# Optimization experiments

Hardware: AMD Instinct MI355X
Metric: run time of the kernel (lower is better)

The kernel has to match this reference:

```python
import jax, jax.numpy as jnp
import numpy as np

H = 256
L = 3
LN_EPS = 1e-5


def _layernorm(z, g, b):
    mu = jnp.mean(z, axis=-1, keepdims=True)
    var = jnp.mean(jnp.square(z - mu), axis=-1, keepdims=True)
    return (z - mu) / jnp.sqrt(var + LN_EPS) * g + b


def setup_inputs() -> dict:
    key = jax.random.key(0)
    ks = jax.random.split(key, 32)
    B, n = 32, 1024
    N = B * n
    E = 16 * N
    node_in, edge_in = 3, 4
    s = 0.05
    inp = {
        'x': jax.random.normal(ks[0], (N, node_in), jnp.float32),
        'edge_attr': jax.random.normal(ks[1], (E, edge_in), jnp.float32),
        'edge_index': jax.random.randint(ks[2], (2, E), 0, N, jnp.int64),
        'a': jax.random.randint(ks[3], (B, n), 0, 2, jnp.int32),
        # node_proj: Linear(node_in+1 -> H)
        'np_w': jax.random.normal(ks[4], (node_in + 1, H), jnp.float32) * s,
        'np_b': jnp.zeros((H,), jnp.float32),
        # edge_mlp: Linear(edge_in->H), ReLU, Linear(H->H)
        'em_w1': jax.random.normal(ks[5], (edge_in, H), jnp.float32) * s,
        'em_b1': jnp.zeros((H,), jnp.float32),
        'em_w2': jax.random.normal(ks[6], (H, H), jnp.float32) * s,
        'em_b2': jnp.zeros((H,), jnp.float32),
        # per-layer GINEConv internal edge lin (edge_dim=H -> H)
        'lin_w': jax.random.normal(ks[7], (L, H, H), jnp.float32) * s,
        'lin_b': jnp.zeros((L, H), jnp.float32),
        # per-layer GINEConv nn: Linear(H->H), ReLU, Linear(H->H)
        'm_w1': jax.random.normal(ks[8], (L, H, H), jnp.float32) * s,
        'm_b1': jnp.zeros((L, H), jnp.float32),
        'm_w2': jax.random.normal(ks[9], (L, H, H), jnp.float32) * s,
        'm_b2': jnp.zeros((L, H), jnp.float32),
        # per-layer LayerNorm
        'ln_g': jnp.ones((L, H), jnp.float32),
        'ln_b': jnp.zeros((L, H), jnp.float32),
        # head: Linear(H->H), ReLU, Linear(H->1)
        'hd_w1': jax.random.normal(ks[10], (H, H), jnp.float32) * s,
        'hd_b1': jnp.zeros((H,), jnp.float32),
        'hd_w2': jax.random.normal(ks[11], (H, 1), jnp.float32) * s,
        'hd_b2': jnp.zeros((1,), jnp.float32),
    }
    return inp


def reference(x, edge_attr, edge_index, a,
              np_w, np_b, em_w1, em_b1, em_w2, em_b2,
              lin_w, lin_b, m_w1, m_b1, m_w2, m_b2, ln_g, ln_b,
              hd_w1, hd_b1, hd_w2, hd_b2):
    N = x.shape[0]
    B, n = a.shape
    # graphs are packed contiguously: batch = i//n, local = i%n ->
    # a[batch, local] == a.reshape(-1)
    a_s = a.reshape(-1).astype(x.dtype)[:, None]            # [N,1]
    h = jax.nn.relu(jnp.concatenate([x, a_s], -1) @ np_w + np_b)  # [N,H]
    e = jax.nn.relu(edge_attr @ em_w1 + em_b1) @ em_w2 + em_b2    # [E,H]
    src, dst = edge_index[0], edge_index[1]
    for l in range(L):
        e_l = e @ lin_w[l] + lin_b[l]                       # GINEConv edge lin
        msg = jax.nn.relu(h[src] + e_l)                     # [E,H]
        agg = jax.ops.segment_sum(msg, dst, num_segments=N) # scatter-add
        z = h + agg                                          # (1+eps)*h, eps=0
        z = jax.nn.relu(z @ m_w1[l] + m_b1[l]) @ m_w2[l] + m_b2[l]
        z = _layernorm(z, ln_g[l], ln_b[l])
        h = h + jax.nn.relu(z)                              # residual
    batch_vec = jnp.arange(N) // n
    g = jax.ops.segment_sum(h, batch_vec, num_segments=B) / n  # mean pool
    q = (jax.nn.relu(g @ hd_w1 + hd_b1) @ hd_w2 + hd_b2)[:, 0]
    return q
```

## Files before the change

kernel.cpp:

```cpp
#include <hip/hip_runtime.h>
#include <hip/hip_bf16.h>

#define H 256
#define LN_EPS 1e-5f
#define PITCH 264
#define TE 128

typedef __attribute__((ext_vector_type(8))) short bf16x8;
typedef __attribute__((ext_vector_type(4))) float f32x4;

__device__ __forceinline__ float bf2f(unsigned short u) {
  union { unsigned int i; float f; } v; v.i = ((unsigned int)u) << 16; return v.f;
}
__device__ __forceinline__ unsigned short f2bf(float f) {
  union { float f; unsigned int i; } v; v.f = f;
  unsigned int x = v.i;
  return (unsigned short)((x + 0x7fffu + ((x >> 16) & 1u)) >> 16);
}
__device__ __forceinline__ unsigned int pack2bf(float a, float b) {
  __hip_bfloat162 t = __float22bfloat162_rn(make_float2(a, b));
  unsigned int u;
  __builtin_memcpy(&u, &t, 4);
  return u;
}
__device__ __forceinline__ unsigned short f2bf1(float a) {
  return (unsigned short)pack2bf(a, a);
}
__device__ __forceinline__ void fsplit(float v, unsigned short& hi, unsigned short& lo) {
  hi = f2bf(v);
  lo = f2bf(v - bf2f(hi));
}

__device__ __forceinline__ void gemm_tile(const float* __restrict__ sA,
                                          const float* __restrict__ W,
                                          int lane_j, int rg, float acc[8][4]) {
#pragma unroll
  for (int mm = 0; mm < 8; mm++)
#pragma unroll
    for (int cc = 0; cc < 4; cc++) acc[mm][cc] = 0.f;
  for (int k = 0; k < H; k += 4) {
    float tvf[8][4];
#pragma unroll
    for (int mm = 0; mm < 8; mm++)
      *(float4*)&tvf[mm][0] = *(const float4*)&sA[(rg * 8 + mm) * H + k];
#pragma unroll
    for (int kk = 0; kk < 4; kk++) {
      const float* wr = W + (k + kk) * H + lane_j;
      float w0 = wr[0], w1 = wr[64], w2 = wr[128], w3 = wr[192];
#pragma unroll
      for (int mm = 0; mm < 8; mm++) {
        float av = tvf[mm][kk];
        acc[mm][0] = fmaf(av, w0, acc[mm][0]);
        acc[mm][1] = fmaf(av, w1, acc[mm][1]);
        acc[mm][2] = fmaf(av, w2, acc[mm][2]);
        acc[mm][3] = fmaf(av, w3, acc[mm][3]);
      }
    }
  }
}


__global__ void k_detect(const int* __restrict__ ei, int* __restrict__ flag) {
  if (threadIdx.x == 0 && blockIdx.x == 0)
    *flag = (ei[1] == 0 && ei[3] == 0 && ei[5] == 0 && ei[7] == 0) ? 1 : 0;
}

__global__ __launch_bounds__(256) void k_zero(float4* __restrict__ p, int n4) {
  int i = blockIdx.x * 256 + threadIdx.x;
  if (i < n4) p[i] = make_float4(0.f, 0.f, 0.f, 0.f);
}

__global__ __launch_bounds__(256) void k_hist(
    const void* __restrict__ ei, const int* __restrict__ flag64,
    int* __restrict__ hist, int E) {
  int e = blockIdx.x * 256 + threadIdx.x;
  if (e >= E) return;
  int d = (*flag64) ? (int)((const long long*)ei)[(size_t)E + e]
                    : ((const int*)ei)[(size_t)E + e];
  atomicAdd(&hist[d], 1);
}

__global__ __launch_bounds__(256) void k_scan(
    const int* __restrict__ hist, int* __restrict__ cursor, int N) {
  __shared__ int part[256];
  int tid = threadIdx.x;
  int chunk = (N + 255) / 256;
  int s = 0;
  for (int i = 0; i < chunk; i++) {
    int idx = tid * chunk + i;
    if (idx < N) s += hist[idx];
  }
  part[tid] = s;
  __syncthreads();
  for (int off = 1; off < 256; off <<= 1) {
    int v = (tid >= off) ? part[tid - off] : 0;
    __syncthreads();
    part[tid] += v;
    __syncthreads();
  }
  int excl = (tid == 0) ? 0 : part[tid - 1];
  for (int i = 0; i < chunk; i++) {
    int idx = tid * chunk + i;
    if (idx < N) {
      cursor[idx] = excl;
      excl += hist[idx];
    }
  }
}

__global__ __launch_bounds__(256) void k_scatter(
    const void* __restrict__ ei, const int* __restrict__ flag64,
    const float* __restrict__ ea, int* __restrict__ cursor,
    int* __restrict__ srcS, int* __restrict__ dstS, float* __restrict__ eaS, int E) {
  int e = blockIdx.x * 256 + threadIdx.x;
  if (e >= E) return;
  int is64 = *flag64;
  int s = is64 ? (int)((const long long*)ei)[e] : ((const int*)ei)[e];
  int d = is64 ? (int)((const long long*)ei)[(size_t)E + e]
               : ((const int*)ei)[(size_t)E + e];
  int p = atomicAdd(&cursor[d], 1);
  srcS[p] = s;
  dstS[p] = d;
  ((float4*)eaS)[p] = ((const float4*)ea)[e];
}

__global__ __launch_bounds__(256) void k_node_proj(
    const float* __restrict__ x, const int* __restrict__ a,
    const float* __restrict__ w, const float* __restrict__ b,
    float* __restrict__ h, unsigned short* __restrict__ hbf, int N) {
  int node = blockIdx.x;
  int j = threadIdx.x;
  float acc = b[j];
  acc = fmaf(x[node * 3 + 0], w[0 * H + j], acc);
  acc = fmaf(x[node * 3 + 1], w[1 * H + j], acc);
  acc = fmaf(x[node * 3 + 2], w[2 * H + j], acc);
  acc = fmaf((float)a[node], w[3 * H + j], acc);
  float v = fmaxf(acc, 0.f);
  h[(size_t)node * H + j] = v;
  hbf[(size_t)node * H + j] = f2bf1(v);
}

__global__ __launch_bounds__(256, 2) void k_wcomb(
    const float* __restrict__ w2, const float* __restrict__ lin_w,
    unsigned short* __restrict__ wcTh, unsigned short* __restrict__ wcTl) {
  __shared__ __align__(16) float sA[32 * H];
  int l = blockIdx.x >> 3, tile = blockIdx.x & 7;
  int tid = threadIdx.x;
  const float4* src = (const float4*)(w2 + (size_t)tile * 32 * H);
#pragma unroll
  for (int it = 0; it < 8; it++) {
    int vi = it * 256 + tid;
    *(float4*)&sA[vi * 4] = src[vi];
  }
  __syncthreads();
  int lane_j = tid & 63, rg = tid >> 6;
  float acc[8][4];
  gemm_tile(sA, lin_w + (size_t)l * H * H, lane_j, rg, acc);
  unsigned short* oh = wcTh + (size_t)l * H * H;
  unsigned short* ol = wcTl + (size_t)l * H * H;
#pragma unroll
  for (int cc = 0; cc < 4; cc++) {
    int j = lane_j + 64 * cc;
#pragma unroll
    for (int mm = 0; mm < 8; mm++) {
      int k = tile * 32 + rg * 8 + mm;
      unsigned short hi, lo;
      fsplit(acc[mm][cc], hi, lo);
      oh[(size_t)j * H + k] = hi;
      ol[(size_t)j * H + k] = lo;
    }
  }
}

__global__ __launch_bounds__(256) void k_beta(
    const float* __restrict__ lin_w, const float* __restrict__ lin_b,
    const float* __restrict__ b2, float* __restrict__ beta) {
  int l = blockIdx.x, j = threadIdx.x;
  const float* W = lin_w + (size_t)l * H * H;
  float v = lin_b[l * H + j];
  for (int k = 0; k < H; k++) v = fmaf(b2[k], W[k * H + j], v);
  beta[l * H + j] = v;
}

__global__ __launch_bounds__(256) void k_transp(
    const float* __restrict__ in,
    unsigned short* __restrict__ outh, unsigned short* __restrict__ outl) {
  int l = blockIdx.z;
  int kb = blockIdx.x * 64, nb = blockIdx.y * 64;
  int tid = threadIdx.x;
  __shared__ float T[64][65];
  const float* src = in + (size_t)l * H * H;
#pragma unroll
  for (int it = 0; it < 16; it++) {
    int idx = it * 256 + tid;
    int kl = idx >> 6, nl = idx & 63;
    T[kl][nl] = src[(size_t)(kb + kl) * H + nb + nl];
  }
  __syncthreads();
  unsigned short* dh = outh + (size_t)l * H * H;
  unsigned short* dl = outl + (size_t)l * H * H;
#pragma unroll
  for (int it = 0; it < 8; it++) {
    int u = it * 256 + tid;
    int nl = u >> 5, k2 = (u & 31) * 2;
    unsigned short h0, l0, h1, l1;
    fsplit(T[k2][nl], h0, l0);
    fsplit(T[k2 + 1][nl], h1, l1);
    size_t o = (size_t)(nb + nl) * H + kb + k2;
    *(unsigned int*)&dh[o] = (unsigned int)h0 | ((unsigned int)h1 << 16);
    *(unsigned int*)&dl[o] = (unsigned int)l0 | ((unsigned int)l1 << 16);
  }
}


__global__ __launch_bounds__(1024, 8) void k_edge_mfma(
    const float* __restrict__ eaS,
    const float* __restrict__ w1, const float* __restrict__ b1,
    const unsigned short* __restrict__ Wth,
    const float* __restrict__ beta,
    const unsigned short* __restrict__ hbf, float* __restrict__ agg,
    const int* __restrict__ srcS, const int* __restrict__ dstS) {
  __shared__ __align__(16) unsigned short sAh[TE * PITCH];
  __shared__ __align__(16) float sEA[TE * 4];
  __shared__ int sSrc[TE];
  __shared__ int sDst[TE];
  int tid = threadIdx.x;
  int base = blockIdx.x * TE;
  if (tid < TE) {
    sSrc[tid] = srcS[base + tid];
  } else if (tid < 2 * TE) {
    sDst[tid - TE] = dstS[base + tid - TE];
  } else if (tid < 3 * TE) {
    int t = tid - 2 * TE;
    ((float4*)sEA)[t] = ((const float4*)(eaS + (size_t)base * 4))[t];
  }
  __syncthreads();
  {
    int j2 = (tid & 127) * 2;
    int r0 = (tid >> 7) * 16;
    float wv0[4], wv1[4];
#pragma unroll
    for (int q = 0; q < 4; q++) { wv0[q] = w1[q * H + j2]; wv1[q] = w1[q * H + j2 + 1]; }
    float bb0 = b1[j2], bb1 = b1[j2 + 1];
#pragma unroll
    for (int m = r0; m < r0 + 16; m++) {
      float t0 = bb0, t1 = bb1;
#pragma unroll
      for (int q = 0; q < 4; q++) {
        float eav = sEA[m * 4 + q];
        t0 = fmaf(eav, wv0[q], t0);
        t1 = fmaf(eav, wv1[q], t1);
      }
      *(unsigned int*)&sAh[m * PITCH + j2] = pack2bf(fmaxf(t0, 0.f), fmaxf(t1, 0.f));
    }
  }
  __syncthreads();
  int lane = tid & 63, wv = tid >> 6;
  int lane15 = lane & 15, quad = lane >> 4;
  f32x4 acc[8];
#pragma unroll
  for (int i = 0; i < 8; i++) acc[i] = (f32x4){0.f, 0.f, 0.f, 0.f};
  const unsigned short* aph = sAh + lane15 * PITCH + quad * 8;
  const unsigned short* bph = Wth + (size_t)(wv * 16 + lane15) * H + quad * 8;
#pragma unroll
  for (int st = 0; st < 8; st++) {
    bf16x8 bhf = *(const bf16x8*)(bph + st * 32);
#pragma unroll
    for (int rg = 0; rg < 8; rg++) {
      bf16x8 ah = *(const bf16x8*)(aph + rg * 16 * PITCH + st * 32);
      acc[rg] = __builtin_amdgcn_mfma_f32_16x16x32_bf16(ah, bhf, acc[rg], 0, 0, 0);
    }
  }
  float bv = beta[wv * 16 + lane15];
  __syncthreads();
#pragma unroll
  for (int rg = 0; rg < 8; rg++) {
#pragma unroll
    for (int r = 0; r < 4; r++) {
      int row = rg * 16 + quad * 4 + r;
      sAh[row * PITCH + wv * 16 + lane15] = f2bf1(acc[rg][r] + bv);
    }
  }
  int jcol2 = (tid & 127) * 2, grp = tid >> 7;
  const int* msrc = sSrc + grp * 16;
  unsigned int hvp[16];
#pragma unroll
  for (int m = 0; m < 16; m++)
    hvp[m] = *(const unsigned int*)&hbf[(size_t)msrc[m] * H + jcol2];
  __syncthreads();
  {
    const int* mdst = sDst + grp * 16;
    float run0 = 0.f, run1 = 0.f;
    int prev = mdst[0];
#pragma unroll
    for (int m = 0; m < 16; m++) {
      int d = mdst[m];
      unsigned int hp = hvp[m];
      unsigned int ev = *(const unsigned int*)&sAh[(grp * 16 + m) * PITCH + jcol2];
      if (d != prev) {
        atomicAdd(&agg[(size_t)prev * H + jcol2], run0);
        atomicAdd(&agg[(size_t)prev * H + jcol2 + 1], run1);
        run0 = 0.f; run1 = 0.f;
        prev = d;
      }
      run0 += fmaxf(bf2f((unsigned short)hp) + bf2f((unsigned short)ev), 0.f);
      run1 += fmaxf(bf2f((unsigned short)(hp >> 16)) + bf2f((unsigned short)(ev >> 16)), 0.f);
    }
    atomicAdd(&agg[(size_t)prev * H + jcol2], run0);
    atomicAdd(&agg[(size_t)prev * H + jcol2 + 1], run1);
  }
}

__global__ __launch_bounds__(1024, 8) void k_node_mfma(
    float* __restrict__ h, unsigned short* __restrict__ hbf,
    float* __restrict__ agg,
    const unsigned short* __restrict__ w1Th, const float* __restrict__ b1,
    const unsigned short* __restrict__ w2Th, const float* __restrict__ b2,
    const float* __restrict__ lng, const float* __restrict__ lnb) {
  __shared__ __align__(16) unsigned short sAh[64 * PITCH];
  __shared__ float sPartS[64][16];
  __shared__ float sPartQ[64][16];
  __shared__ float sMu[64];
  __shared__ float sRstd[64];
  int tid = threadIdx.x;
  int base = blockIdx.x * 64;
  const float4* h4 = (const float4*)(h + (size_t)base * H);
  float4* a4 = (float4*)(agg + (size_t)base * H);
#pragma unroll
  for (int it = 0; it < 4; it++) {
    int vi = it * 1024 + tid;
    int row = vi >> 6, c4 = (vi & 63) * 4;
    float4 hv = h4[vi], av = a4[vi];
    a4[vi] = make_float4(0.f, 0.f, 0.f, 0.f);
    uint2 uh;
    uh.x = pack2bf(hv.x + av.x, hv.y + av.y);
    uh.y = pack2bf(hv.z + av.z, hv.w + av.w);
    *(uint2*)&sAh[row * PITCH + c4] = uh;
  }
  __syncthreads();
  int lane = tid & 63, wv = tid >> 6;
  int lane15 = lane & 15, quad = lane >> 4;
  int col = wv * 16 + lane15;
  const unsigned short* aph = sAh + lane15 * PITCH + quad * 8;
  f32x4 acc[4];
#pragma unroll
  for (int i = 0; i < 4; i++) acc[i] = (f32x4){0.f, 0.f, 0.f, 0.f};
  {
    const unsigned short* bph = w1Th + (size_t)col * H + quad * 8;
#pragma unroll
    for (int st = 0; st < 8; st++) {
      bf16x8 bhf = *(const bf16x8*)(bph + st * 32);
#pragma unroll
      for (int rg = 0; rg < 4; rg++) {
        bf16x8 ah = *(const bf16x8*)(aph + rg * 16 * PITCH + st * 32);
        acc[rg] = __builtin_amdgcn_mfma_f32_16x16x32_bf16(ah, bhf, acc[rg], 0, 0, 0);
      }
    }
  }
  float b1v = b1[col];
  __syncthreads();
#pragma unroll
  for (int rg = 0; rg < 4; rg++)
#pragma unroll
    for (int r = 0; r < 4; r++) {
      int row = rg * 16 + quad * 4 + r;
      sAh[row * PITCH + col] = f2bf1(fmaxf(acc[rg][r] + b1v, 0.f));
    }
  __syncthreads();
  f32x4 acc2[4];
#pragma unroll
  for (int i = 0; i < 4; i++) acc2[i] = (f32x4){0.f, 0.f, 0.f, 0.f};
  {
    const unsigned short* bph = w2Th + (size_t)col * H + quad * 8;
#pragma unroll
    for (int st = 0; st < 8; st++) {
      bf16x8 bhf = *(const bf16x8*)(bph + st * 32);
#pragma unroll
      for (int rg = 0; rg < 4; rg++) {
        bf16x8 ah = *(const bf16x8*)(aph + rg * 16 * PITCH + st * 32);
        acc2[rg] = __builtin_amdgcn_mfma_f32_16x16x32_bf16(ah, bhf, acc2[rg], 0, 0, 0);
      }
    }
  }
  float b2v = b2[col], gv = lng[col], bbv = lnb[col];
#pragma unroll
  for (int rg = 0; rg < 4; rg++)
#pragma unroll
    for (int r = 0; r < 4; r++) {
      int row = rg * 16 + quad * 4 + r;
      float z2 = acc2[rg][r] + b2v;
      float s = z2, ss = z2 * z2;
      s += __shfl_xor(s, 1, 64); ss += __shfl_xor(ss, 1, 64);
      s += __shfl_xor(s, 2, 64); ss += __shfl_xor(ss, 2, 64);
      s += __shfl_xor(s, 4, 64); ss += __shfl_xor(ss, 4, 64);
      s += __shfl_xor(s, 8, 64); ss += __shfl_xor(ss, 8, 64);
      if (lane15 == 0) { sPartS[row][wv] = s; sPartQ[row][wv] = ss; }
    }
  __syncthreads();
  if (tid < 64) {
    float s = 0.f, ss = 0.f;
#pragma unroll
    for (int w = 0; w < 16; w++) { s += sPartS[tid][w]; ss += sPartQ[tid][w]; }
    float mu = s * (1.f / H);
    float var = ss * (1.f / H) - mu * mu;
    sMu[tid] = mu;
    sRstd[tid] = rsqrtf(var + LN_EPS);
  }
  __syncthreads();
#pragma unroll
  for (int rg = 0; rg < 4; rg++)
#pragma unroll
    for (int r = 0; r < 4; r++) {
      int row = rg * 16 + quad * 4 + r;
      float mu = sMu[row], rstd = sRstd[row];
      size_t o = (size_t)(base + row) * H + col;
      float z2 = acc2[rg][r] + b2v;
      float v = fmaf((z2 - mu) * rstd, gv, bbv);
      float hn = h[o] + fmaxf(v, 0.f);
      h[o] = hn;
      hbf[o] = f2bf1(hn);
    }
}

__global__ __launch_bounds__(256) void k_pool(
    const float* __restrict__ h, float* __restrict__ g, int n) {
  int tid = threadIdx.x;
  int row0 = blockIdx.x * 64;
  int b = row0 / n;
  const float* hb = h + (size_t)row0 * H;
  float s0 = 0.f, s1 = 0.f, s2 = 0.f, s3 = 0.f;
  for (int i = 0; i < 64; i += 4) {
    s0 += hb[(size_t)(i + 0) * H + tid];
    s1 += hb[(size_t)(i + 1) * H + tid];
    s2 += hb[(size_t)(i + 2) * H + tid];
    s3 += hb[(size_t)(i + 3) * H + tid];
  }
  atomicAdd(&g[(size_t)b * H + tid], s0 + s1 + s2 + s3);
}

__global__ __launch_bounds__(256) void k_head(
    const float* __restrict__ g,
    const float* __restrict__ w1, const float* __restrict__ b1,
    const float* __restrict__ w2, const float* __restrict__ b2,
    float* __restrict__ out, int n) {
  __shared__ float sG[H];
  __shared__ float sT[H];
  __shared__ float sR[4];
  int b = blockIdx.x, tid = threadIdx.x;
  sG[tid] = g[(size_t)b * H + tid] / (float)n;
  __syncthreads();
  float t = b1[tid];
  for (int k = 0; k < H; k++) t = fmaf(sG[k], w1[k * H + tid], t);
  sT[tid] = fmaxf(t, 0.f);
  __syncthreads();
  float p = sT[tid] * w2[tid];
#pragma unroll
  for (int off = 32; off > 0; off >>= 1) p += __shfl_xor(p, off, 64);
  if ((tid & 63) == 0) sR[tid >> 6] = p;
  __syncthreads();
  if (tid == 0) out[b] = sR[0] + sR[1] + sR[2] + sR[3] + b2[0];
}

extern "C" void kernel_launch(void* const* d_in, const int* in_sizes, int n_in,
                              void* d_out, int out_size, void* d_ws, size_t ws_size,
                              hipStream_t stream) {
  const float* x      = (const float*)d_in[0];
  const float* ea     = (const float*)d_in[1];
  const void*  ei     = d_in[2];
  const int*   a      = (const int*)d_in[3];
  const float* np_w   = (const float*)d_in[4];
  const float* np_b   = (const float*)d_in[5];
  const float* em_w1  = (const float*)d_in[6];
  const float* em_b1  = (const float*)d_in[7];
  const float* em_w2  = (const float*)d_in[8];
  const float* em_b2  = (const float*)d_in[9];
  const float* lin_w  = (const float*)d_in[10];
  const float* lin_b  = (const float*)d_in[11];
  const float* m_w1   = (const float*)d_in[12];
  const float* m_b1   = (const float*)d_in[13];
  const float* m_w2   = (const float*)d_in[14];
  const float* m_b2   = (const float*)d_in[15];
  const float* ln_g   = (const float*)d_in[16];
  const float* ln_b   = (const float*)d_in[17];
  const float* hd_w1  = (const float*)d_in[18];
  const float* hd_b1  = (const float*)d_in[19];
  const float* hd_w2  = (const float*)d_in[20];
  const float* hd_b2  = (const float*)d_in[21];

  int N = in_sizes[0] / 3;
  int E = in_sizes[1] / 4;
  int B = out_size;
  int n = N / B;

  char* ws = (char*)d_ws;
  size_t off = 0;
  auto alloc = [&](size_t bytes) {
    char* p = ws + off;
    off += (bytes + 255) & ~(size_t)255;
    return p;
  };
  float* h    = (float*)alloc((size_t)N * H * 4);
  unsigned short* hbf = (unsigned short*)alloc((size_t)N * H * 2);
  float* agg  = (float*)alloc((size_t)N * H * 4);
  unsigned short* wcTh = (unsigned short*)alloc((size_t)3 * H * H * 2);
  unsigned short* wcTl = (unsigned short*)alloc((size_t)3 * H * H * 2);
  unsigned short* w1Th = (unsigned short*)alloc((size_t)3 * H * H * 2);
  unsigned short* w1Tl = (unsigned short*)alloc((size_t)3 * H * H * 2);
  unsigned short* w2Th = (unsigned short*)alloc((size_t)3 * H * H * 2);
  unsigned short* w2Tl = (unsigned short*)alloc((size_t)3 * H * H * 2);
  float* beta  = (float*)alloc(3 * H * 4);
  int*   flag  = (int*)alloc(4);
  int*   hist  = (int*)alloc((size_t)N * 4);
  int*   curs  = (int*)alloc((size_t)N * 4);
  int*   srcS  = (int*)alloc((size_t)E * 4);
  int*   dstS  = (int*)alloc((size_t)E * 4);
  float* eaS   = (float*)alloc((size_t)E * 4 * 4);
  float* g     = (float*)alloc((size_t)B * H * 4);

  float* out = (float*)d_out;
  int ebl = (E + 255) / 256;

  k_detect<<<1, 64, 0, stream>>>((const int*)ei, flag);
  k_zero<<<(N + 1023) / 1024, 256, 0, stream>>>((float4*)hist, N / 4);
  k_hist<<<ebl, 256, 0, stream>>>(ei, flag, hist, E);
  k_scan<<<1, 256, 0, stream>>>(hist, curs, N);
  k_scatter<<<ebl, 256, 0, stream>>>(ei, flag, ea, curs, srcS, dstS, eaS, E);
  k_node_proj<<<N, 256, 0, stream>>>(x, a, np_w, np_b, h, hbf, N);
  k_wcomb<<<24, 256, 0, stream>>>(em_w2, lin_w, wcTh, wcTl);
  k_beta<<<3, 256, 0, stream>>>(lin_w, lin_b, em_b2, beta);
  k_transp<<<dim3(4, 4, 3), 256, 0, stream>>>(m_w1, w1Th, w1Tl);
  k_transp<<<dim3(4, 4, 3), 256, 0, stream>>>(m_w2, w2Th, w2Tl);

  int n4 = N * H / 4;
  k_zero<<<(n4 + 255) / 256, 256, 0, stream>>>((float4*)agg, n4);
  for (int l = 0; l < 3; l++) {
    k_edge_mfma<<<E / TE, 1024, 0, stream>>>(eaS, em_w1, em_b1,
                                             wcTh + (size_t)l * H * H,
                                             beta + (size_t)l * H,
                                             hbf, agg, srcS, dstS);
    k_node_mfma<<<N / 64, 1024, 0, stream>>>(h, hbf, agg,
                                             w1Th + (size_t)l * H * H,
                                             m_b1 + (size_t)l * H,
                                             w2Th + (size_t)l * H * H,
                                             m_b2 + (size_t)l * H,
                                             ln_g + (size_t)l * H, ln_b + (size_t)l * H);
  }
  int g4 = B * H / 4;
  k_zero<<<(g4 + 255) / 256, 256, 0, stream>>>((float4*)g, g4);
  k_pool<<<N / 64, 256, 0, stream>>>(h, g, n);
  k_head<<<B, 256, 0, stream>>>(g, hd_w1, hd_b1, hd_w2, hd_b2, out, n);
}
```

Measured before the change: 879.3 us.

## Fuse mean-pool into last node layer, drop unused lo-split weights, restripe gather columns

Pooling moves into the final node-MLP kernel, which atomically accumulates per-graph sums instead of writing h and launching a separate pool kernel. The unused low-half bf16 weight splits are removed so the preprocessing kernels write less. In the edge kernel the gather and atomics now cover columns j and j+128 instead of two adjacent columns, and the edge-attr load is vectorised. The agg zeroing moves out of the node kernel into a separate k_zero launch per layer, which adds three full-buffer memset passes in exchange for removing the stores from the node kernel.

```diff
diff --git a/kernel.cpp b/kernel.cpp
--- a/kernel.cpp
+++ b/kernel.cpp
@@ -11,11 +11,6 @@
 
 __device__ __forceinline__ float bf2f(unsigned short u) {
   union { unsigned int i; float f; } v; v.i = ((unsigned int)u) << 16; return v.f;
-}
-__device__ __forceinline__ unsigned short f2bf(float f) {
-  union { float f; unsigned int i; } v; v.f = f;
-  unsigned int x = v.i;
-  return (unsigned short)((x + 0x7fffu + ((x >> 16) & 1u)) >> 16);
 }
 __device__ __forceinline__ unsigned int pack2bf(float a, float b) {
   __hip_bfloat162 t = __float22bfloat162_rn(make_float2(a, b));
@@ -25,10 +20,6 @@
 }
 __device__ __forceinline__ unsigned short f2bf1(float a) {
   return (unsigned short)pack2bf(a, a);
-}
-__device__ __forceinline__ void fsplit(float v, unsigned short& hi, unsigned short& lo) {
-  hi = f2bf(v);
-  lo = f2bf(v - bf2f(hi));
 }
 
 __device__ __forceinline__ void gemm_tile(const float* __restrict__ sA,
@@ -142,7 +133,7 @@
 
 __global__ __launch_bounds__(256, 2) void k_wcomb(
     const float* __restrict__ w2, const float* __restrict__ lin_w,
-    unsigned short* __restrict__ wcTh, unsigned short* __restrict__ wcTl) {
+    unsigned short* __restrict__ wcTh) {
   __shared__ __align__(16) float sA[32 * H];
   int l = blockIdx.x >> 3, tile = blockIdx.x & 7;
   int tid = threadIdx.x;
@@ -157,17 +148,13 @@
   float acc[8][4];
   gemm_tile(sA, lin_w + (size_t)l * H * H, lane_j, rg, acc);
   unsigned short* oh = wcTh + (size_t)l * H * H;
-  unsigned short* ol = wcTl + (size_t)l * H * H;
 #pragma unroll
   for (int cc = 0; cc < 4; cc++) {
     int j = lane_j + 64 * cc;
 #pragma unroll
     for (int mm = 0; mm < 8; mm++) {
       int k = tile * 32 + rg * 8 + mm;
-      unsigned short hi, lo;
-      fsplit(acc[mm][cc], hi, lo);
-      oh[(size_t)j * H + k] = hi;
-      ol[(size_t)j * H + k] = lo;
+      oh[(size_t)j * H + k] = f2bf1(acc[mm][cc]);
     }
   }
 }
@@ -183,8 +170,7 @@
 }
 
 __global__ __launch_bounds__(256) void k_transp(
-    const float* __restrict__ in,
-    unsigned short* __restrict__ outh, unsigned short* __restrict__ outl) {
+    const float* __restrict__ in, unsigned short* __restrict__ outh) {
   int l = blockIdx.z;
   int kb = blockIdx.x * 64, nb = blockIdx.y * 64;
   int tid = threadIdx.x;
@@ -198,17 +184,12 @@
   }
   __syncthreads();
   unsigned short* dh = outh + (size_t)l * H * H;
-  unsigned short* dl = outl + (size_t)l * H * H;
 #pragma unroll
   for (int it = 0; it < 8; it++) {
     int u = it * 256 + tid;
     int nl = u >> 5, k2 = (u & 31) * 2;
-    unsigned short h0, l0, h1, l1;
-    fsplit(T[k2][nl], h0, l0);
-    fsplit(T[k2 + 1][nl], h1, l1);
     size_t o = (size_t)(nb + nl) * H + kb + k2;
-    *(unsigned int*)&dh[o] = (unsigned int)h0 | ((unsigned int)h1 << 16);
-    *(unsigned int*)&dl[o] = (unsigned int)l0 | ((unsigned int)l1 << 16);
+    *(unsigned int*)&dh[o] = pack2bf(T[k2][nl], T[k2 + 1][nl]);
   }
 }
 
@@ -244,13 +225,12 @@
     float bb0 = b1[j2], bb1 = b1[j2 + 1];
 #pragma unroll
     for (int m = r0; m < r0 + 16; m++) {
-      float t0 = bb0, t1 = bb1;
-#pragma unroll
-      for (int q = 0; q < 4; q++) {
-        float eav = sEA[m * 4 + q];
-        t0 = fmaf(eav, wv0[q], t0);
-        t1 = fmaf(eav, wv1[q], t1);
-      }
+      float4 e4 = *(const float4*)&sEA[m * 4];
+      float t0 = fmaf(e4.x, wv0[0], bb0);
+      float t1 = fmaf(e4.x, wv1[0], bb1);
+      t0 = fmaf(e4.y, wv0[1], t0);  t1 = fmaf(e4.y, wv1[1], t1);
+      t0 = fmaf(e4.z, wv0[2], t0);  t1 = fmaf(e4.z, wv1[2], t1);
+      t0 = fmaf(e4.w, wv0[3], t0);  t1 = fmaf(e4.w, wv1[3], t1);
       *(unsigned int*)&sAh[m * PITCH + j2] = pack2bf(fmaxf(t0, 0.f), fmaxf(t1, 0.f));
     }
   }
@@ -281,42 +261,48 @@
       sAh[row * PITCH + wv * 16 + lane15] = f2bf1(acc[rg][r] + bv);
     }
   }
-  int jcol2 = (tid & 127) * 2, grp = tid >> 7;
+  int jA = tid & 127, grp = tid >> 7;
   const int* msrc = sSrc + grp * 16;
-  unsigned int hvp[16];
-#pragma unroll
-  for (int m = 0; m < 16; m++)
-    hvp[m] = *(const unsigned int*)&hbf[(size_t)msrc[m] * H + jcol2];
+  unsigned int hp[16];
+#pragma unroll
+  for (int m = 0; m < 16; m++) {
+    unsigned int a = hbf[(size_t)msrc[m] * H + jA];
+    unsigned int b = hbf[(size_t)msrc[m] * H + jA + 128];
+    hp[m] = a | (b << 16);
+  }
   __syncthreads();
   {
     const int* mdst = sDst + grp * 16;
-    float run0 = 0.f, run1 = 0.f;
+    float runA = 0.f, runB = 0.f;
     int prev = mdst[0];
 #pragma unroll
     for (int m = 0; m < 16; m++) {
       int d = mdst[m];
-      unsigned int hp = hvp[m];
-      unsigned int ev = *(const unsigned int*)&sAh[(grp * 16 + m) * PITCH + jcol2];
+      int row = grp * 16 + m;
+      unsigned short evA = sAh[row * PITCH + jA];
+      unsigned short evB = sAh[row * PITCH + jA + 128];
       if (d != prev) {
-        atomicAdd(&agg[(size_t)prev * H + jcol2], run0);
-        atomicAdd(&agg[(size_t)prev * H + jcol2 + 1], run1);
-        run0 = 0.f; run1 = 0.f;
+        atomicAdd(&agg[(size_t)prev * H + jA], runA);
+        atomicAdd(&agg[(size_t)prev * H + jA + 128], runB);
+        runA = 0.f; runB = 0.f;
         prev = d;
       }
-      run0 += fmaxf(bf2f((unsigned short)hp) + bf2f((unsigned short)ev), 0.f);
-      run1 += fmaxf(bf2f((unsigned short)(hp >> 16)) + bf2f((unsigned short)(ev >> 16)), 0.f);
-    }
-    atomicAdd(&agg[(size_t)prev * H + jcol2], run0);
-    atomicAdd(&agg[(size_t)prev * H + jcol2 + 1], run1);
+      unsigned int h2 = hp[m];
+      runA += fmaxf(bf2f((unsigned short)h2) + bf2f(evA), 0.f);
+      runB += fmaxf(bf2f((unsigned short)(h2 >> 16)) + bf2f(evB), 0.f);
+    }
+    atomicAdd(&agg[(size_t)prev * H + jA], runA);
+    atomicAdd(&agg[(size_t)prev * H + jA + 128], runB);
   }
 }
 
 __global__ __launch_bounds__(1024, 8) void k_node_mfma(
     float* __restrict__ h, unsigned short* __restrict__ hbf,
-    float* __restrict__ agg,
+    const float* __restrict__ agg,
     const unsigned short* __restrict__ w1Th, const float* __restrict__ b1,
     const unsigned short* __restrict__ w2Th, const float* __restrict__ b2,
-    const float* __restrict__ lng, const float* __restrict__ lnb) {
+    const float* __restrict__ lng, const float* __restrict__ lnb,
+    float* __restrict__ g, int n, int last) {
   __shared__ __align__(16) unsigned short sAh[64 * PITCH];
   __shared__ float sPartS[64][16];
   __shared__ float sPartQ[64][16];
@@ -325,13 +311,12 @@
   int tid = threadIdx.x;
   int base = blockIdx.x * 64;
   const float4* h4 = (const float4*)(h + (size_t)base * H);
-  float4* a4 = (float4*)(agg + (size_t)base * H);
+  const float4* a4 = (const float4*)(agg + (size_t)base * H);
 #pragma unroll
   for (int it = 0; it < 4; it++) {
     int vi = it * 1024 + tid;
     int row = vi >> 6, c4 = (vi & 63) * 4;
     float4 hv = h4[vi], av = a4[vi];
-    a4[vi] = make_float4(0.f, 0.f, 0.f, 0.f);
     uint2 uh;
     uh.x = pack2bf(hv.x + av.x, hv.y + av.y);
     uh.y = pack2bf(hv.z + av.z, hv.w + av.w);
@@ -407,35 +392,36 @@
     sRstd[tid] = rsqrtf(var + LN_EPS);
   }
   __syncthreads();
-#pragma unroll
-  for (int rg = 0; rg < 4; rg++)
-#pragma unroll
-    for (int r = 0; r < 4; r++) {
-      int row = rg * 16 + quad * 4 + r;
-      float mu = sMu[row], rstd = sRstd[row];
-      size_t o = (size_t)(base + row) * H + col;
-      float z2 = acc2[rg][r] + b2v;
-      float v = fmaf((z2 - mu) * rstd, gv, bbv);
-      float hn = h[o] + fmaxf(v, 0.f);
-      h[o] = hn;
-      hbf[o] = f2bf1(hn);
-    }
-}
-
-__global__ __launch_bounds__(256) void k_pool(
-    const float* __restrict__ h, float* __restrict__ g, int n) {
-  int tid = threadIdx.x;
-  int row0 = blockIdx.x * 64;
-  int b = row0 / n;
-  const float* hb = h + (size_t)row0 * H;
-  float s0 = 0.f, s1 = 0.f, s2 = 0.f, s3 = 0.f;
-  for (int i = 0; i < 64; i += 4) {
-    s0 += hb[(size_t)(i + 0) * H + tid];
-    s1 += hb[(size_t)(i + 1) * H + tid];
-    s2 += hb[(size_t)(i + 2) * H + tid];
-    s3 += hb[(size_t)(i + 3) * H + tid];
-  }
-  atomicAdd(&g[(size_t)b * H + tid], s0 + s1 + s2 + s3);
+  if (!last) {
+#pragma unroll
+    for (int rg = 0; rg < 4; rg++)
+#pragma unroll
+      for (int r = 0; r < 4; r++) {
+        int row = rg * 16 + quad * 4 + r;
+        float mu = sMu[row], rstd = sRstd[row];
+        size_t o = (size_t)(base + row) * H + col;
+        float z2 = acc2[rg][r] + b2v;
+        float v = fmaf((z2 - mu) * rstd, gv, bbv);
+        float hn = h[o] + fmaxf(v, 0.f);
+        h[o] = hn;
+        hbf[o] = f2bf1(hn);
+      }
+  } else {
+    int bg = base / n;
+    float psum = 0.f;
+#pragma unroll
+    for (int rg = 0; rg < 4; rg++)
+#pragma unroll
+      for (int r = 0; r < 4; r++) {
+        int row = rg * 16 + quad * 4 + r;
+        float mu = sMu[row], rstd = sRstd[row];
+        size_t o = (size_t)(base + row) * H + col;
+        float z2 = acc2[rg][r] + b2v;
+        float v = fmaf((z2 - mu) * rstd, gv, bbv);
+        psum += h[o] + fmaxf(v, 0.f);
+      }
+    atomicAdd(&g[(size_t)bg * H + col], psum);
+  }
 }
 
 __global__ __launch_bounds__(256) void k_head(
@@ -503,11 +489,8 @@
   unsigned short* hbf = (unsigned short*)alloc((size_t)N * H * 2);
   float* agg  = (float*)alloc((size_t)N * H * 4);
   unsigned short* wcTh = (unsigned short*)alloc((size_t)3 * H * H * 2);
-  unsigned short* wcTl = (unsigned short*)alloc((size_t)3 * H * H * 2);
   unsigned short* w1Th = (unsigned short*)alloc((size_t)3 * H * H * 2);
-  unsigned short* w1Tl = (unsigned short*)alloc((size_t)3 * H * H * 2);
   unsigned short* w2Th = (unsigned short*)alloc((size_t)3 * H * H * 2);
-  unsigned short* w2Tl = (unsigned short*)alloc((size_t)3 * H * H * 2);
   float* beta  = (float*)alloc(3 * H * 4);
   int*   flag  = (int*)alloc(4);
   int*   hist  = (int*)alloc((size_t)N * 4);
@@ -526,14 +509,16 @@
   k_scan<<<1, 256, 0, stream>>>(hist, curs, N);
   k_scatter<<<ebl, 256, 0, stream>>>(ei, flag, ea, curs, srcS, dstS, eaS, E);
   k_node_proj<<<N, 256, 0, stream>>>(x, a, np_w, np_b, h, hbf, N);
-  k_wcomb<<<24, 256, 0, stream>>>(em_w2, lin_w, wcTh, wcTl);
+  k_wcomb<<<24, 256, 0, stream>>>(em_w2, lin_w, wcTh);
   k_beta<<<3, 256, 0, stream>>>(lin_w, lin_b, em_b2, beta);
-  k_transp<<<dim3(4, 4, 3), 256, 0, stream>>>(m_w1, w1Th, w1Tl);
-  k_transp<<<dim3(4, 4, 3), 256, 0, stream>>>(m_w2, w2Th, w2Tl);
+  k_transp<<<dim3(4, 4, 3), 256, 0, stream>>>(m_w1, w1Th);
+  k_transp<<<dim3(4, 4, 3), 256, 0, stream>>>(m_w2, w2Th);
 
   int n4 = N * H / 4;
-  k_zero<<<(n4 + 255) / 256, 256, 0, stream>>>((float4*)agg, n4);
+  int g4 = B * H / 4;
+  k_zero<<<(g4 + 255) / 256, 256, 0, stream>>>((float4*)g, g4);
   for (int l = 0; l < 3; l++) {
+    k_zero<<<(n4 + 255) / 256, 256, 0, stream>>>((float4*)agg, n4);
     k_edge_mfma<<<E / TE, 1024, 0, stream>>>(eaS, em_w1, em_b1,
                                              wcTh + (size_t)l * H * H,
                                              beta + (size_t)l * H,
@@ -543,10 +528,8 @@
                                              m_b1 + (size_t)l * H,
                                              w2Th + (size_t)l * H * H,
                                              m_b2 + (size_t)l * H,
-                                             ln_g + (size_t)l * H, ln_b + (size_t)l * H);
-  }
-  int g4 = B * H / 4;
-  k_zero<<<(g4 + 255) / 256, 256, 0, stream>>>((float4*)g, g4);
-  k_pool<<<N / 64, 256, 0, stream>>>(h, g, n);
+                                             ln_g + (size_t)l * H, ln_b + (size_t)l * H,
+                                             g, n, (l == 2) ? 1 : 0);
+  }
   k_head<<<B, 256, 0, stream>>>(g, hd_w1, hd_b1, hd_w2, hd_b2, out, n);
 }
```

Result: no change. 881.9 us (+0.3%).
